# Kernel tuning notes

Hardware: AMD Instinct MI355X
Metric: run time of the kernel (lower is better)

Reference implementation:

```python
import jax, jax.numpy as jnp
import numpy as np

# Fuzzy convolution (gaussian membership, 'prod' T-norm):
# firing_r(patch) = prod_{ki,kj,c} exp(-0.5*((x-mu_{r,c})*sigma_{ki,kj,c,r})^2)
#                 = exp(-0.5 * sum_{ki,kj,c} ((x-mu)*sigma)^2)
# The quadratic expands so the whole premise stage is two VALID convolutions:
#   sum (x^2)*s2 - 2*sum x*(mu*s2) + sum (mu^2)*s2,  with s2 = sigma^2.

_DN = ('NHWC', 'HWIO', 'NHWC')

def _conv(a, k):
    return jax.lax.conv_general_dilated(a, k, window_strides=(1, 1), padding='VALID', dimension_numbers=_DN)

def _firing(x, sigma, mu):
    # x: (B,H,W,C); sigma: (kh,kw,C,R); mu: (R,C)
    s2 = sigma * sigma                              # (kh,kw,C,R)
    mu_cr = mu.T[None, None, :, :]                  # (1,1,C,R)
    quad = _conv(x * x, s2) - 2.0 * _conv(x, s2 * mu_cr)  # (B,H',W',R)
    const = jnp.sum(s2 * mu_cr * mu_cr, axis=(0, 1, 2))   # (R,)
    return jnp.exp(-0.5 * (quad + const))           # (B,H',W',R)

def setup_inputs() -> dict:
    key = jax.random.key(0)
    k1, k2, k3, k4 = jax.random.split(key, 4)
    B, H, W, C = 32, 256, 256, 32
    R, O = 8, 16
    x = jax.random.normal(k1, (B, H, W, C), dtype=jnp.float32)
    # small positive sigmas keep sum over 3*3*32 window terms O(1) so firing is not ~0
    premise_sigma = 0.1 * jax.random.uniform(k2, (3, 3, C, R), dtype=jnp.float32)
    premise_mu = jax.random.normal(k3, (R, C), dtype=jnp.float32)
    residual = jnp.full((1,), 0.01, dtype=jnp.float32)  # Constant(0.01) initializer
    consequent_bias = jax.random.normal(k4, (R + 1, O), dtype=jnp.float32)
    return {"x": x, "premise_sigma": premise_sigma, "premise_mu": premise_mu,
            "residual": residual, "consequent_bias": consequent_bias}

def reference(x, premise_sigma, premise_mu, residual, consequent_bias):
    phi = _firing(x, premise_sigma, premise_mu)                     # (B,H',W',R)
    res = jnp.broadcast_to(residual, phi.shape[:-1] + (1,))         # residual rule
    phi = jnp.concatenate([phi, res], axis=-1)                      # (B,H',W',R+1)
    phi_norm = phi / (jnp.sum(phi, axis=-1, keepdims=True) + 1e-9)  # normalized firing
    # constant-output-MF consequent combine: rules -> outputs
    return jnp.einsum('bhwr,ro->bhwo', phi_norm, consequent_bias)   # (B,H',W',O)
```

## Files before the change

kernel.cpp:

```cpp
#include <hip/hip_runtime.h>


#define CIN 32
#define HH  256
#define WW  256
#define HO  254
#define WO  254
#define BB  32
#define OO  16

#define TW 64
#define TH 8
#define LROWS 10
#define LPIX 66
#define ROWCH (LPIX * 4)
#define LDS_CHUNKS (LROWS * ROWCH)
#define ACH (6 * ROWCH)
#define AIT 7
#define BIT 5
#define NTILE (4 * 32 * BB)

typedef _Float16 half8 __attribute__((ext_vector_type(8)));
typedef _Float16 half2v __attribute__((ext_vector_type(2)));
typedef float f32x4 __attribute__((ext_vector_type(4)));

static __device__ __forceinline__ unsigned short f2h(float f) {
    _Float16 h = (_Float16)f;
    return *reinterpret_cast<unsigned short*>(&h);
}

static __device__ __forceinline__ half8 pack_pkrtz(const float4& a, const float4& b) {
    uint4 u;
    u.x = __builtin_bit_cast(unsigned, __builtin_amdgcn_cvt_pkrtz(a.x, a.y));
    u.y = __builtin_bit_cast(unsigned, __builtin_amdgcn_cvt_pkrtz(a.z, a.w));
    u.z = __builtin_bit_cast(unsigned, __builtin_amdgcn_cvt_pkrtz(b.x, b.y));
    u.w = __builtin_bit_cast(unsigned, __builtin_amdgcn_cvt_pkrtz(b.z, b.w));
    return __builtin_bit_cast(half8, u);
}

__global__ __launch_bounds__(256) void prep_kernel(const float* __restrict__ sigma,
                                                   const float* __restrict__ mu,
                                                   unsigned short* __restrict__ wb,
                                                   float* __restrict__ Kc) {
    const int tid = threadIdx.x;
    for (int item = tid; item < 18 * 64; item += 256) {
        const int frag = item >> 6;
        const int lane = item & 63;
        const int tap = frag >> 1, ftype = frag & 1;
        const int n = lane & 15, g = lane >> 4;
#pragma unroll
        for (int e = 0; e < 8; ++e) {
            float wgt = 0.f;
            if (n < 8) {
                const int c = g * 8 + e;
                const float sg = sigma[(tap * CIN + c) * 8 + n];
                const float s2 = sg * sg;
                wgt = ftype ? -0.5f * s2 : s2 * mu[n * CIN + c];
            }
            wb[item * 8 + e] = f2h(wgt);
        }
    }
    if (tid < 8) {
        const int r = tid;
        float k = 0.f;
        for (int item = 0; item < 9 * CIN; ++item) {
            const int c = item & 31;
            const float sg = sigma[item * 8 + r];
            const float m = mu[r * CIN + c];
            k = fmaf(sg * sg, m * m, k);
        }
        Kc[r] = -0.5f * k;
    }
}

__global__ __launch_bounds__(256, 3) void fuzzy_main(const float* __restrict__ x,
                                                     const unsigned short* __restrict__ wb,
                                                     const float* __restrict__ Kc,
                                                     const float* __restrict__ residual,
                                                     const float* __restrict__ cb,
                                                     float* __restrict__ out) {
    __shared__ __align__(16) unsigned char ldsRaw[LDS_CHUNKS * 16];
    half8* ldsH = reinterpret_cast<half8*>(ldsRaw);

    const int tid = threadIdx.x;
    const int lin  = blockIdx.x;
    const int tile = ((lin & 7) << 9) | (lin >> 3);
    const int jt = tile & 3;
    const int it = (tile >> 2) & 31;
    const int b  = tile >> 7;
    const int i0 = min(TH * it, HO - TH);
    const int j0 = min(TW * jt, WO - TW);

    const float4* xbase = reinterpret_cast<const float4*>(
        x + (((size_t)b * HH + (size_t)i0) * WW + (size_t)j0) * CIN);

    float4 va[AIT], vb[AIT];
#pragma unroll
    for (int t = 0; t < AIT; ++t) {
        const int f = min(tid + t * 256, ACH - 1);
        const int row = f / ROWCH, rem = f - row * ROWCH;
        va[t] = xbase[(size_t)row * 2048 + 2 * rem];
        vb[t] = xbase[(size_t)row * 2048 + 2 * rem + 1];
    }
    float4 wa[BIT], wbv4[BIT];
#pragma unroll
    for (int t = 0; t < BIT; ++t) {
        const int f = min(ACH + tid + t * 256, LDS_CHUNKS - 1);
        const int row = f / ROWCH, rem = f - row * ROWCH;
        wa[t] = xbase[(size_t)row * 2048 + 2 * rem];
        wbv4[t] = xbase[(size_t)row * 2048 + 2 * rem + 1];
    }

#pragma unroll
    for (int t = 0; t < AIT; ++t) {
        const int f = tid + t * 256;
        if (f < ACH) {
            const int row = f / ROWCH, rem = f - row * ROWCH;
            const int px = rem >> 2, gg = rem & 3;
            ldsH[row * ROWCH + (px << 2) + (gg ^ (px & 3))] = pack_pkrtz(va[t], vb[t]);
        }
    }

    const int lane = tid & 63;
    const int m = lane & 15, g = lane >> 4;

    const half8* wbp = reinterpret_cast<const half8*>(wb);
    half8 Bf[18];
#pragma unroll
    for (int q = 0; q < 18; ++q) Bf[q] = wbp[q * 64 + lane];

    const float res = residual[0];
    const float4 kc4 = reinterpret_cast<const float4*>(Kc)[g & 1];
    half8 a2;
#pragma unroll
    for (int e = 0; e < 8; ++e) {
        const int r = g * 8 + e;
        const float w = cb[min(r, 8) * OO + m];
        a2[e] = (_Float16)((r <= 8) ? w : 0.f);
    }
    unsigned resw;
    { unsigned short rb = f2h(res); resw = (unsigned)rb; }

    __syncthreads();

    const int wv_ = tid >> 6;

    int bc[3];
#pragma unroll
    for (int kj = 0; kj < 3; ++kj) {
        const int p = m + kj;
        bc[kj] = (p << 2) + (g ^ (p & 3));
    }

#pragma unroll
    for (int half = 0; half < 2; ++half) {
        const int row0 = wv_ + 4 * half;

        f32x4 acc[4];
#pragma unroll
        for (int nt = 0; nt < 4; ++nt) acc[nt] = (f32x4){0.f, 0.f, 0.f, 0.f};

        const half8* baseS = ldsH + row0 * ROWCH;
#pragma unroll
        for (int ki = 0; ki < 3; ++ki) {
#pragma unroll
            for (int kj = 0; kj < 3; ++kj) {
                const int tap = ki * 3 + kj;
                half8 ax[4];
#pragma unroll
                for (int nt = 0; nt < 4; ++nt)
                    ax[nt] = baseS[ki * ROWCH + nt * 64 + bc[kj]];
#pragma unroll
                for (int nt = 0; nt < 4; ++nt)
                    acc[nt] = __builtin_amdgcn_mfma_f32_16x16x32_f16(Bf[2 * tap], ax[nt], acc[nt], 0, 0, 0);
#pragma unroll
                for (int nt = 0; nt < 4; ++nt) {
                    const half8 ax2 = ax[nt] * ax[nt];
                    acc[nt] = __builtin_amdgcn_mfma_f32_16x16x32_f16(Bf[2 * tap + 1], ax2, acc[nt], 0, 0, 0);
                }
            }
        }

        if (half == 0) {
#pragma unroll
            for (int t = 0; t < BIT; ++t) {
                const int f = ACH + tid + t * 256;
                if (f < LDS_CHUNKS) {
                    const int row = f / ROWCH, rem = f - row * ROWCH;
                    const int px = rem >> 2, gg = rem & 3;
                    ldsH[row * ROWCH + (px << 2) + (gg ^ (px & 3))] = pack_pkrtz(wa[t], wbv4[t]);
                }
            }
        }

        const size_t orow = ((size_t)b * HO + (size_t)(i0 + row0)) * WO + (size_t)j0;
#pragma unroll
        for (int nt = 0; nt < 4; ++nt) {
            float phv[4];
#pragma unroll
            for (int e = 0; e < 4; ++e) {
                const float t = __expf(acc[nt][e] + ((const float*)&kc4)[e]);
                phv[e] = (g < 2) ? t : 0.f;
            }
            const float S = (phv[0] + phv[1]) + (phv[2] + phv[3]);
            const float T = S + __shfl_xor(S, 16);
            const float denom = T + __shfl_xor(T, 32) + res + 1e-9f;
            const float inv = __builtin_amdgcn_rcpf(denom);

            const unsigned w01 = (unsigned)f2h(phv[0]) | ((unsigned)f2h(phv[1]) << 16);
            const unsigned w23 = (unsigned)f2h(phv[2]) | ((unsigned)f2h(phv[3]) << 16);
            const unsigned p01 = __shfl_xor(w01, 16);
            const unsigned p23 = __shfl_xor(w23, 16);
            uint4 bw;
            bw.x = (g == 0) ? w01 : ((g == 1) ? resw : 0u);
            bw.y = (g == 0) ? w23 : 0u;
            bw.z = (g == 0) ? p01 : 0u;
            bw.w = (g == 0) ? p23 : 0u;
            const half8 b2 = __builtin_bit_cast(half8, bw);

            f32x4 acc2 = (f32x4){0.f, 0.f, 0.f, 0.f};
            acc2 = __builtin_amdgcn_mfma_f32_16x16x32_f16(a2, b2, acc2, 0, 0, 0);

            f32x4 v;
            v[0] = acc2[0] * inv; v[1] = acc2[1] * inv;
            v[2] = acc2[2] * inv; v[3] = acc2[3] * inv;
            float* op = out + (orow + (size_t)(nt * 16 + m)) * OO + g * 4;
            __builtin_nontemporal_store(v, reinterpret_cast<f32x4*>(op));
        }

        if (half == 0) __syncthreads();
    }
}

extern "C" void kernel_launch(void* const* d_in, const int* in_sizes, int n_in,
                              void* d_out, int out_size, void* d_ws, size_t ws_size,
                              hipStream_t stream) {
    const float* x     = (const float*)d_in[0];
    const float* sigma = (const float*)d_in[1];
    const float* mu    = (const float*)d_in[2];
    const float* resid = (const float*)d_in[3];
    const float* cb    = (const float*)d_in[4];
    float* outp = (float*)d_out;

    float* Kc = (float*)d_ws;
    unsigned short* wb = (unsigned short*)(Kc + 8);

    hipLaunchKernelGGL(prep_kernel, dim3(1), dim3(256), 0, stream, sigma, mu, wb, Kc);
    hipLaunchKernelGGL(fuzzy_main, dim3(NTILE), dim3(256), 0, stream,
                       x, wb, Kc, resid, cb, outp);
}
```

Before: 104.0 us.

## Shrink row tiles to 7 rows, stage all input at once, raise occupancy

```diff
diff --git a/kernel.cpp b/kernel.cpp
--- a/kernel.cpp
+++ b/kernel.cpp
@@ -10,18 +10,17 @@
 #define OO  16
 
 #define TW 64
-#define TH 8
-#define LROWS 10
+#define TH 7
+#define LROWS 9
 #define LPIX 66
 #define ROWCH (LPIX * 4)
 #define LDS_CHUNKS (LROWS * ROWCH)
-#define ACH (6 * ROWCH)
-#define AIT 7
-#define BIT 5
-#define NTILE (4 * 32 * BB)
+#define STAGE_ITERS 10
+#define NBAND 37
+#define NTILE (4 * NBAND * BB)
+#define CPX (NTILE / 8)
 
 typedef _Float16 half8 __attribute__((ext_vector_type(8)));
-typedef _Float16 half2v __attribute__((ext_vector_type(2)));
 typedef float f32x4 __attribute__((ext_vector_type(4)));
 
 static __device__ __forceinline__ unsigned short f2h(float f) {
@@ -73,7 +72,7 @@
     }
 }
 
-__global__ __launch_bounds__(256, 3) void fuzzy_main(const float* __restrict__ x,
+__global__ __launch_bounds__(256, 4) void fuzzy_main(const float* __restrict__ x,
                                                      const unsigned short* __restrict__ wb,
                                                      const float* __restrict__ Kc,
                                                      const float* __restrict__ residual,
@@ -84,37 +83,29 @@
 
     const int tid = threadIdx.x;
     const int lin  = blockIdx.x;
-    const int tile = ((lin & 7) << 9) | (lin >> 3);
-    const int jt = tile & 3;
-    const int it = (tile >> 2) & 31;
-    const int b  = tile >> 7;
+    const int tile = (lin & 7) * CPX + (lin >> 3);
+    const int jt   = tile & 3;
+    const int rest = tile >> 2;
+    const int it   = rest % NBAND;
+    const int b    = rest / NBAND;
     const int i0 = min(TH * it, HO - TH);
     const int j0 = min(TW * jt, WO - TW);
 
     const float4* xbase = reinterpret_cast<const float4*>(
         x + (((size_t)b * HH + (size_t)i0) * WW + (size_t)j0) * CIN);
 
-    float4 va[AIT], vb[AIT];
-#pragma unroll
-    for (int t = 0; t < AIT; ++t) {
-        const int f = min(tid + t * 256, ACH - 1);
+    float4 va[STAGE_ITERS], vb[STAGE_ITERS];
+#pragma unroll
+    for (int t = 0; t < STAGE_ITERS; ++t) {
+        const int f = min(tid + t * 256, LDS_CHUNKS - 1);
         const int row = f / ROWCH, rem = f - row * ROWCH;
         va[t] = xbase[(size_t)row * 2048 + 2 * rem];
         vb[t] = xbase[(size_t)row * 2048 + 2 * rem + 1];
     }
-    float4 wa[BIT], wbv4[BIT];
-#pragma unroll
-    for (int t = 0; t < BIT; ++t) {
-        const int f = min(ACH + tid + t * 256, LDS_CHUNKS - 1);
-        const int row = f / ROWCH, rem = f - row * ROWCH;
-        wa[t] = xbase[(size_t)row * 2048 + 2 * rem];
-        wbv4[t] = xbase[(size_t)row * 2048 + 2 * rem + 1];
-    }
-
-#pragma unroll
-    for (int t = 0; t < AIT; ++t) {
+#pragma unroll
+    for (int t = 0; t < STAGE_ITERS; ++t) {
         const int f = tid + t * 256;
-        if (f < ACH) {
+        if (f < LDS_CHUNKS) {
             const int row = f / ROWCH, rem = f - row * ROWCH;
             const int px = rem >> 2, gg = rem & 3;
             ldsH[row * ROWCH + (px << 2) + (gg ^ (px & 3))] = pack_pkrtz(va[t], vb[t]);
@@ -152,10 +143,7 @@
         bc[kj] = (p << 2) + (g ^ (p & 3));
     }
 
-#pragma unroll
-    for (int half = 0; half < 2; ++half) {
-        const int row0 = wv_ + 4 * half;
-
+    auto compute_row = [&](int row0) {
         f32x4 acc[4];
 #pragma unroll
         for (int nt = 0; nt < 4; ++nt) acc[nt] = (f32x4){0.f, 0.f, 0.f, 0.f};
@@ -177,18 +165,6 @@
                 for (int nt = 0; nt < 4; ++nt) {
                     const half8 ax2 = ax[nt] * ax[nt];
                     acc[nt] = __builtin_amdgcn_mfma_f32_16x16x32_f16(Bf[2 * tap + 1], ax2, acc[nt], 0, 0, 0);
-                }
-            }
-        }
-
-        if (half == 0) {
-#pragma unroll
-            for (int t = 0; t < BIT; ++t) {
-                const int f = ACH + tid + t * 256;
-                if (f < LDS_CHUNKS) {
-                    const int row = f / ROWCH, rem = f - row * ROWCH;
-                    const int px = rem >> 2, gg = rem & 3;
-                    ldsH[row * ROWCH + (px << 2) + (gg ^ (px & 3))] = pack_pkrtz(wa[t], wbv4[t]);
                 }
             }
         }
@@ -227,9 +203,10 @@
             float* op = out + (orow + (size_t)(nt * 16 + m)) * OO + g * 4;
             __builtin_nontemporal_store(v, reinterpret_cast<f32x4*>(op));
         }
-
-        if (half == 0) __syncthreads();
-    }
+    };
+
+    compute_row(wv_);
+    if (wv_ < 3) compute_row(4 + wv_);
 }
 
 extern "C" void kernel_launch(void* const* d_in, const int* in_sizes, int n_in,
```

Result: slower. 118.2 us (+13.6%).
